# Optimization experiments

Hardware: AMD Instinct MI355X
Metric: run time of the kernel (lower is better)

The kernel has to match this reference:

```python
import jax, jax.numpy as jnp
import numpy as np

BATCH = 2048
INPUT_SIZE = 2048
OUTPUT_SIZE = 2048
N_INPUTS = 6            # fan-in per LUT node
K = 1 << N_INPUTS       # 64 table entries per node


def setup_inputs() -> dict:
    key = jax.random.key(0)
    k1, k2, k3 = jax.random.split(key, 3)
    x = jax.random.uniform(k1, (BATCH, INPUT_SIZE), dtype=jnp.float32)
    table = jax.random.normal(k2, (OUTPUT_SIZE, K), dtype=jnp.float32)
    mapping = jax.random.randint(k3, (OUTPUT_SIZE, N_INPUTS), 0, INPUT_SIZE, dtype=jnp.int64)
    return {"x": x, "table": table, "mapping": mapping}


def reference(x, table, mapping):
    # x: (B, I) in [0,1]; table: (O, 2^n) raw logits; mapping: (O, n) int indices
    O, n = mapping.shape
    Kv = 1 << n
    # per-node input gather -> (B, O, n)
    xg = x[:, mapping]
    # binary codes of the 2^n LUT vertices: bits[k, i] = i-th bit of k
    bits = ((jnp.arange(Kv)[:, None] >> jnp.arange(n)[None, :]) & 1).astype(x.dtype)  # (K, n)
    # vertex probabilities prod_i (x_i if bit else 1-x_i), built by a tiny fixed loop over n
    probs = jnp.ones((x.shape[0], O, Kv), dtype=x.dtype)
    for i in range(n):
        xi = xg[:, :, i][:, :, None]                      # (B, O, 1)
        bi = bits[:, i][None, None, :]                    # (1, 1, K)
        probs = probs * (xi * bi + (1.0 - xi) * (1.0 - bi))
    # differentiable LUT lookup: expected table value under vertex distribution
    out = jnp.einsum('bok,ok->bo', probs, jax.nn.sigmoid(table))  # (B, O)
    return out
```

## Files before the change

kernel.cpp:

```cpp
#include <hip/hip_runtime.h>
#include <math.h>

#define B_TOTAL 2048
#define I_TOTAL 2048
#define O_TOTAL 2048
#define KW 64
#define NIN 6
#define BLOCK 256
#define TILE_B 16
#define CH 4
#define BBLOCKS (B_TOTAL / TILE_B)
#define OBLOCKS (O_TOTAL / BLOCK)

__global__ void prep_kernel(const float* __restrict__ table,
                            const unsigned int* __restrict__ map_raw,
                            float* __restrict__ wT,
                            int* __restrict__ m32T)
{
    int idx = blockIdx.x * blockDim.x + threadIdx.x;
    int o = idx >> 6, k = idx & 63;
    float s = 1.0f / (1.0f + __expf(-table[idx]));
    float v;
    if (k >= 32) {
        float s0 = 1.0f / (1.0f + __expf(-table[idx - 32]));
        v = s - s0;
    } else {
        v = s;
    }
    wT[k * O_TOTAL + o] = v;

    if (idx < O_TOTAL * NIN) {
        bool is64 = ((map_raw[1] | map_raw[3] | map_raw[5] | map_raw[7]) == 0u);
        int val = is64 ? (int)map_raw[2 * idx] : (int)map_raw[idx];
        int oo = idx / NIN, ii = idx - oo * NIN;
        m32T[ii * O_TOTAL + oo] = val;
    }
}

__global__ __launch_bounds__(BLOCK) void lut_main(
    const float* __restrict__ x,
    const float* __restrict__ wT,
    const int*   __restrict__ m32T,
    float*       __restrict__ out)
{
    __shared__ float xs[CH * I_TOTAL];

    const int o  = blockIdx.y * BLOCK + threadIdx.x;
    const int b0 = blockIdx.x * TILE_B;

    float ww[KW];
    #pragma unroll
    for (int k = 0; k < KW; ++k) ww[k] = wT[k * O_TOTAL + o];

    int m[NIN];
    #pragma unroll
    for (int i = 0; i < NIN; ++i) m[i] = m32T[i * O_TOTAL + o];

    #pragma unroll
    for (int c = 0; c < TILE_B / CH; ++c) {
        __syncthreads();
        const float4* src = (const float4*)(x + (size_t)(b0 + c * CH) * I_TOTAL);
        float4* dst = (float4*)xs;
        #pragma unroll
        for (int t = 0; t < (CH * I_TOTAL / 4) / BLOCK; ++t)
            dst[t * BLOCK + threadIdx.x] = src[t * BLOCK + threadIdx.x];
        __syncthreads();

        #pragma unroll
        for (int cr = 0; cr < CH; ++cr) {
            const float* xr = xs + cr * I_TOTAL;
            float xv[NIN];
            #pragma unroll
            for (int i = 0; i < NIN; ++i) xv[i] = xr[m[i]];

            float t[32];
            #pragma unroll
            for (int j = 0; j < 32; ++j) t[j] = fmaf(xv[5], ww[j + 32], ww[j]);
            #pragma unroll
            for (int j = 0; j < 16; ++j) t[j] = fmaf(xv[4], t[j + 16] - t[j], t[j]);
            #pragma unroll
            for (int j = 0; j < 8;  ++j) t[j] = fmaf(xv[3], t[j + 8]  - t[j], t[j]);
            #pragma unroll
            for (int j = 0; j < 4;  ++j) t[j] = fmaf(xv[2], t[j + 4]  - t[j], t[j]);
            #pragma unroll
            for (int j = 0; j < 2;  ++j) t[j] = fmaf(xv[1], t[j + 2]  - t[j], t[j]);
            float res = fmaf(xv[0], t[1] - t[0], t[0]);

            out[(size_t)(b0 + c * CH + cr) * O_TOTAL + o] = res;
        }
    }
}

extern "C" void kernel_launch(void* const* d_in, const int* in_sizes, int n_in,
                              void* d_out, int out_size, void* d_ws, size_t ws_size,
                              hipStream_t stream)
{
    const float*        x       = (const float*)d_in[0];
    const float*        table   = (const float*)d_in[1];
    const unsigned int* map_raw = (const unsigned int*)d_in[2];
    float* out  = (float*)d_out;
    float* wT   = (float*)d_ws;
    int*   m32T = (int*)((char*)d_ws + (size_t)O_TOTAL * KW * sizeof(float));

    prep_kernel<<<(O_TOTAL * KW) / BLOCK, BLOCK, 0, stream>>>(table, map_raw, wT, m32T);

    dim3 grid(BBLOCKS, OBLOCKS);
    lut_main<<<grid, dim3(BLOCK), 0, stream>>>(x, wT, m32T, out);
}
```

Baseline: 84.29 us.

## Transpose x and output so each wave handles one LUT node across batch

Adds a tiled transpose kernel that lays x out column-major, so each wave owns one output node and its lanes cover consecutive batch rows. The gathers become coalesced global loads from xT rows instead of LDS lookups, the per-node weights load uniformly across the wave, and the result is written to a transposed buffer and then transposed back. This drops the shared-memory staging of x and its barriers. In exchange it adds two full-matrix transposes (about 16 MB each of read plus write) and extra workspace.

Result: slower. 95.84 us (+13.7%).

```diff
diff --git a/kernel.cpp b/kernel.cpp
--- a/kernel.cpp
+++ b/kernel.cpp
@@ -7,87 +7,102 @@
 #define KW 64
 #define NIN 6
 #define BLOCK 256
-#define TILE_B 16
-#define CH 4
-#define BBLOCKS (B_TOTAL / TILE_B)
-#define OBLOCKS (O_TOTAL / BLOCK)
+
+#define WS_SIGW 0
+#define WS_M32  (512 * 1024)
+#define WS_XT   (1024 * 1024)
+#define WS_OUTT (WS_XT + B_TOTAL * I_TOTAL * 4)
 
 __global__ void prep_kernel(const float* __restrict__ table,
                             const unsigned int* __restrict__ map_raw,
-                            float* __restrict__ wT,
-                            int* __restrict__ m32T)
+                            float* __restrict__ sigw,
+                            int* __restrict__ m32)
 {
     int idx = blockIdx.x * blockDim.x + threadIdx.x;
-    int o = idx >> 6, k = idx & 63;
+    int k = idx & 63;
     float s = 1.0f / (1.0f + __expf(-table[idx]));
-    float v;
+    float v = s;
     if (k >= 32) {
         float s0 = 1.0f / (1.0f + __expf(-table[idx - 32]));
         v = s - s0;
-    } else {
-        v = s;
     }
-    wT[k * O_TOTAL + o] = v;
+    sigw[idx] = v;
 
     if (idx < O_TOTAL * NIN) {
         bool is64 = ((map_raw[1] | map_raw[3] | map_raw[5] | map_raw[7]) == 0u);
-        int val = is64 ? (int)map_raw[2 * idx] : (int)map_raw[idx];
-        int oo = idx / NIN, ii = idx - oo * NIN;
-        m32T[ii * O_TOTAL + oo] = val;
+        m32[idx] = is64 ? (int)map_raw[2 * idx] : (int)map_raw[idx];
+    }
+}
+
+__global__ __launch_bounds__(256) void transpose_k(const float* __restrict__ src,
+                                                   float* __restrict__ dst)
+{
+    __shared__ float tile[64][65];
+    const int t  = threadIdx.x;
+    const int r0 = blockIdx.y * 64;
+    const int c0 = blockIdx.x * 64;
+    const int rr = t >> 4;
+    const int cc = (t & 15) << 2;
+    #pragma unroll
+    for (int p = 0; p < 4; ++p) {
+        int r = p * 16 + rr;
+        float4 v = *(const float4*)(src + (size_t)(r0 + r) * 2048 + c0 + cc);
+        tile[r][cc + 0] = v.x; tile[r][cc + 1] = v.y;
+        tile[r][cc + 2] = v.z; tile[r][cc + 3] = v.w;
+    }
+    __syncthreads();
+    #pragma unroll
+    for (int p = 0; p < 4; ++p) {
+        int r = p * 16 + rr;
+        float4 v;
+        v.x = tile[cc + 0][r]; v.y = tile[cc + 1][r];
+        v.z = tile[cc + 2][r]; v.w = tile[cc + 3][r];
+        *(float4*)(dst + (size_t)(c0 + r) * 2048 + r0 + cc) = v;
     }
 }
 
 __global__ __launch_bounds__(BLOCK) void lut_main(
-    const float* __restrict__ x,
-    const float* __restrict__ wT,
-    const int*   __restrict__ m32T,
-    float*       __restrict__ out)
+    const float* __restrict__ xT,
+    const float* __restrict__ sigw,
+    const int*   __restrict__ m32,
+    float*       __restrict__ outT)
 {
-    __shared__ float xs[CH * I_TOTAL];
-
-    const int o  = blockIdx.y * BLOCK + threadIdx.x;
-    const int b0 = blockIdx.x * TILE_B;
+    const int wave = threadIdx.x >> 6;
+    const int lane = threadIdx.x & 63;
+    const int o    = blockIdx.y * 4 + wave;
+    const int b0   = blockIdx.x * 512;
 
     float ww[KW];
+    const float* wp = sigw + (size_t)o * KW;
     #pragma unroll
-    for (int k = 0; k < KW; ++k) ww[k] = wT[k * O_TOTAL + o];
+    for (int k = 0; k < KW; ++k) ww[k] = wp[k];
 
     int m[NIN];
     #pragma unroll
-    for (int i = 0; i < NIN; ++i) m[i] = m32T[i * O_TOTAL + o];
+    for (int i = 0; i < NIN; ++i) m[i] = m32[o * NIN + i];
 
     #pragma unroll
-    for (int c = 0; c < TILE_B / CH; ++c) {
-        __syncthreads();
-        const float4* src = (const float4*)(x + (size_t)(b0 + c * CH) * I_TOTAL);
-        float4* dst = (float4*)xs;
+    for (int p = 0; p < 8; ++p) {
+        const int b = b0 + p * 64 + lane;
+        float xv[NIN];
         #pragma unroll
-        for (int t = 0; t < (CH * I_TOTAL / 4) / BLOCK; ++t)
-            dst[t * BLOCK + threadIdx.x] = src[t * BLOCK + threadIdx.x];
-        __syncthreads();
+        for (int i = 0; i < NIN; ++i)
+            xv[i] = xT[(size_t)m[i] * B_TOTAL + b];
 
+        float t[32];
         #pragma unroll
-        for (int cr = 0; cr < CH; ++cr) {
-            const float* xr = xs + cr * I_TOTAL;
-            float xv[NIN];
-            #pragma unroll
-            for (int i = 0; i < NIN; ++i) xv[i] = xr[m[i]];
+        for (int j = 0; j < 32; ++j) t[j] = fmaf(xv[5], ww[j + 32], ww[j]);
+        #pragma unroll
+        for (int j = 0; j < 16; ++j) t[j] = fmaf(xv[4], t[j + 16] - t[j], t[j]);
+        #pragma unroll
+        for (int j = 0; j < 8;  ++j) t[j] = fmaf(xv[3], t[j + 8]  - t[j], t[j]);
+        #pragma unroll
+        for (int j = 0; j < 4;  ++j) t[j] = fmaf(xv[2], t[j + 4]  - t[j], t[j]);
+        #pragma unroll
+        for (int j = 0; j < 2;  ++j) t[j] = fmaf(xv[1], t[j + 2]  - t[j], t[j]);
+        float res = fmaf(xv[0], t[1] - t[0], t[0]);
 
-            float t[32];
-            #pragma unroll
-            for (int j = 0; j < 32; ++j) t[j] = fmaf(xv[5], ww[j + 32], ww[j]);
-            #pragma unroll
-            for (int j = 0; j < 16; ++j) t[j] = fmaf(xv[4], t[j + 16] - t[j], t[j]);
-            #pragma unroll
-            for (int j = 0; j < 8;  ++j) t[j] = fmaf(xv[3], t[j + 8]  - t[j], t[j]);
-            #pragma unroll
-            for (int j = 0; j < 4;  ++j) t[j] = fmaf(xv[2], t[j + 4]  - t[j], t[j]);
-            #pragma unroll
-            for (int j = 0; j < 2;  ++j) t[j] = fmaf(xv[1], t[j + 2]  - t[j], t[j]);
-            float res = fmaf(xv[0], t[1] - t[0], t[0]);
-
-            out[(size_t)(b0 + c * CH + cr) * O_TOTAL + o] = res;
-        }
+        outT[(size_t)o * B_TOTAL + b] = res;
     }
 }
 
@@ -99,11 +114,15 @@
     const float*        table   = (const float*)d_in[1];
     const unsigned int* map_raw = (const unsigned int*)d_in[2];
     float* out  = (float*)d_out;
-    float* wT   = (float*)d_ws;
-    int*   m32T = (int*)((char*)d_ws + (size_t)O_TOTAL * KW * sizeof(float));
+    float* sigw = (float*)((char*)d_ws + WS_SIGW);
+    int*   m32  = (int*)  ((char*)d_ws + WS_M32);
+    float* xT   = (float*)((char*)d_ws + WS_XT);
+    float* outT = (float*)((char*)d_ws + WS_OUTT);
 
-    prep_kernel<<<(O_TOTAL * KW) / BLOCK, BLOCK, 0, stream>>>(table, map_raw, wT, m32T);
+    prep_kernel<<<(O_TOTAL * KW) / BLOCK, BLOCK, 0, stream>>>(table, map_raw, sigw, m32);
+    transpose_k<<<dim3(32, 32), BLOCK, 0, stream>>>(x, xT);
 
-    dim3 grid(BBLOCKS, OBLOCKS);
-    lut_main<<<grid, dim3(BLOCK), 0, stream>>>(x, wT, m32T, out);
+    lut_main<<<dim3(4, 512), BLOCK, 0, stream>>>(xT, sigw, m32, outT);
+
+    transpose_k<<<dim3(32, 32), BLOCK, 0, stream>>>(outT, out);
 }
```

## Pack LUT weights as float2 pairs and reverse multilinear reduction order

Applied to the files above, without the earlier changes.

Reorganizes the precomputed sigmoid table into float2 pairs (value, difference) along bit 0, so the first interpolation level reads adjacent entries as one vector load. The reduction tree is now nested depth-first from xv[0] up to xv[5], which keeps fewer temporaries live at once. It also adds a min-blocks-per-CU hint of 4 to launch_bounds and drops the unroll on the chunk loop, both aimed at lowering register pressure and raising occupancy. The trade-offs are possible register spills under the tighter bound and extra loop overhead from the rolled outer loop.

Result: slower. 86.04 us (+2.1%).

```diff
diff --git a/kernel.cpp b/kernel.cpp
--- a/kernel.cpp
+++ b/kernel.cpp
@@ -12,22 +12,22 @@
 #define BBLOCKS (B_TOTAL / TILE_B)
 #define OBLOCKS (O_TOTAL / BLOCK)
 
+typedef __attribute__((ext_vector_type(2))) float f2;
+
+#define WS_WP  0
+#define WS_M32 (32 * O_TOTAL * sizeof(f2))
+
 __global__ void prep_kernel(const float* __restrict__ table,
                             const unsigned int* __restrict__ map_raw,
-                            float* __restrict__ wT,
+                            f2* __restrict__ wP,
                             int* __restrict__ m32T)
 {
     int idx = blockIdx.x * blockDim.x + threadIdx.x;
-    int o = idx >> 6, k = idx & 63;
-    float s = 1.0f / (1.0f + __expf(-table[idx]));
-    float v;
-    if (k >= 32) {
-        float s0 = 1.0f / (1.0f + __expf(-table[idx - 32]));
-        v = s - s0;
-    } else {
-        v = s;
-    }
-    wT[k * O_TOTAL + o] = v;
+    int o = idx >> 5, j = idx & 31;
+    float s0 = 1.0f / (1.0f + __expf(-table[o * KW + 2 * j]));
+    float s1 = 1.0f / (1.0f + __expf(-table[o * KW + 2 * j + 1]));
+    f2 v; v.x = s0; v.y = s1 - s0;
+    wP[j * O_TOTAL + o] = v;
 
     if (idx < O_TOTAL * NIN) {
         bool is64 = ((map_raw[1] | map_raw[3] | map_raw[5] | map_raw[7]) == 0u);
@@ -37,9 +37,9 @@
     }
 }
 
-__global__ __launch_bounds__(BLOCK) void lut_main(
+__global__ __launch_bounds__(BLOCK, 4) void lut_main(
     const float* __restrict__ x,
-    const float* __restrict__ wT,
+    const f2*    __restrict__ wP,
     const int*   __restrict__ m32T,
     float*       __restrict__ out)
 {
@@ -48,15 +48,14 @@
     const int o  = blockIdx.y * BLOCK + threadIdx.x;
     const int b0 = blockIdx.x * TILE_B;
 
-    float ww[KW];
+    f2 ww[32];
     #pragma unroll
-    for (int k = 0; k < KW; ++k) ww[k] = wT[k * O_TOTAL + o];
+    for (int j = 0; j < 32; ++j) ww[j] = wP[j * O_TOTAL + o];
 
     int m[NIN];
     #pragma unroll
     for (int i = 0; i < NIN; ++i) m[i] = m32T[i * O_TOTAL + o];
 
-    #pragma unroll
     for (int c = 0; c < TILE_B / CH; ++c) {
         __syncthreads();
         const float4* src = (const float4*)(x + (size_t)(b0 + c * CH) * I_TOTAL);
@@ -73,18 +72,34 @@
             #pragma unroll
             for (int i = 0; i < NIN; ++i) xv[i] = xr[m[i]];
 
-            float t[32];
+            float a5[2];
             #pragma unroll
-            for (int j = 0; j < 32; ++j) t[j] = fmaf(xv[5], ww[j + 32], ww[j]);
-            #pragma unroll
-            for (int j = 0; j < 16; ++j) t[j] = fmaf(xv[4], t[j + 16] - t[j], t[j]);
-            #pragma unroll
-            for (int j = 0; j < 8;  ++j) t[j] = fmaf(xv[3], t[j + 8]  - t[j], t[j]);
-            #pragma unroll
-            for (int j = 0; j < 4;  ++j) t[j] = fmaf(xv[2], t[j + 4]  - t[j], t[j]);
-            #pragma unroll
-            for (int j = 0; j < 2;  ++j) t[j] = fmaf(xv[1], t[j + 2]  - t[j], t[j]);
-            float res = fmaf(xv[0], t[1] - t[0], t[0]);
+            for (int h5 = 0; h5 < 2; ++h5) {
+                float a4[2];
+                #pragma unroll
+                for (int h4 = 0; h4 < 2; ++h4) {
+                    float a3[2];
+                    #pragma unroll
+                    for (int h3 = 0; h3 < 2; ++h3) {
+                        float a2[2];
+                        #pragma unroll
+                        for (int h2 = 0; h2 < 2; ++h2) {
+                            float a1[2];
+                            #pragma unroll
+                            for (int h1 = 0; h1 < 2; ++h1) {
+                                int j = (((h5 * 2 + h4) * 2 + h3) * 2 + h2) * 2 + h1;
+                                f2 w = ww[j];
+                                a1[h1] = fmaf(xv[0], w.y, w.x);
+                            }
+                            a2[h2] = fmaf(xv[1], a1[1] - a1[0], a1[0]);
+                        }
+                        a3[h3] = fmaf(xv[2], a2[1] - a2[0], a2[0]);
+                    }
+                    a4[h4] = fmaf(xv[3], a3[1] - a3[0], a3[0]);
+                }
+                a5[h5] = fmaf(xv[4], a4[1] - a4[0], a4[0]);
+            }
+            float res = fmaf(xv[5], a5[1] - a5[0], a5[0]);
 
             out[(size_t)(b0 + c * CH + cr) * O_TOTAL + o] = res;
         }
@@ -99,11 +114,11 @@
     const float*        table   = (const float*)d_in[1];
     const unsigned int* map_raw = (const unsigned int*)d_in[2];
     float* out  = (float*)d_out;
-    float* wT   = (float*)d_ws;
-    int*   m32T = (int*)((char*)d_ws + (size_t)O_TOTAL * KW * sizeof(float));
+    f2*    wP   = (f2*) ((char*)d_ws + WS_WP);
+    int*   m32T = (int*)((char*)d_ws + WS_M32);
 
-    prep_kernel<<<(O_TOTAL * KW) / BLOCK, BLOCK, 0, stream>>>(table, map_raw, wT, m32T);
+    prep_kernel<<<(O_TOTAL * KW / 2) / BLOCK, BLOCK, 0, stream>>>(table, map_raw, wP, m32T);
 
     dim3 grid(BBLOCKS, OBLOCKS);
-    lut_main<<<grid, dim3(BLOCK), 0, stream>>>(x, wT, m32T, out);
+    lut_main<<<grid, dim3(BLOCK), 0, stream>>>(x, wP, m32T, out);
 }
```
